# Optimization experiments

Hardware: AMD Instinct MI355X
Metric: run time of the kernel (lower is better)

Reference implementation:

```python
import jax, jax.numpy as jnp
import numpy as np

FP8_MAX = 448.0  # max representable magnitude of float8_e4m3fn


def _quantize_tensorwise(x):
    """Tensor-wise fp8 quantization. Returns (fp8 tensor, inverse_scale) where
    dequant = fp8.astype(f32) * inverse_scale (matches Fp8Quantization.quantize_tensorwise)."""
    amax = jnp.max(jnp.abs(x))
    inv_scale = jnp.maximum(amax / FP8_MAX, jnp.float32(1e-12))
    q = (x / inv_scale).astype(jnp.float8_e4m3fn)
    return q, inv_scale


def _fp8_mm(qa, qb, sa, sb):
    # scaled fp8 GEMM: accumulate in f32, apply product of per-tensor inverse scales
    return (qa.astype(jnp.float32) @ qb.astype(jnp.float32)) * (sa * sb)


def setup_inputs() -> dict:
    key = jax.random.key(0)
    k1, k2, k3 = jax.random.split(key, 3)
    x = jax.random.normal(k1, (4, 2048, 2048), dtype=jnp.float32)
    weight = jax.random.normal(k2, (2048, 2048), dtype=jnp.float32) * 0.02
    bias = jax.random.normal(k3, (2048,), dtype=jnp.float32) * 0.01
    return {"x": x, "weight": weight, "bias": bias}


def reference(x, weight, bias):
    # flatten leading dims: inputmat = input.view(-1, K)
    K = x.shape[-1]
    xm = x.reshape(-1, K)                      # [T, K]
    qx, sx = _quantize_tensorwise(xm)          # fp8 input + inverse scale
    qwt, swt = _quantize_tensorwise(weight.T)  # fp8 weight^T [K, N] + inverse scale
    out = _fp8_mm(qx, qwt, sx, swt) + bias     # [T, N]
    return out.reshape(*x.shape[:-1], -1)
```

## Files before the change

### kernel.cpp

```cpp
#include <hip/hip_runtime.h>
#include <stdint.h>

typedef float f32x4 __attribute__((ext_vector_type(4)));
typedef int   i32x4 __attribute__((ext_vector_type(4)));
typedef int   i32x8 __attribute__((ext_vector_type(8)));

__global__ __launch_bounds__(256) void amax2_kernel(
    const float* __restrict__ x, int nx4,
    const float* __restrict__ w, int nw4,
    int xblocks, int* __restrict__ out) {
  const float4* src;
  int n4, j0, stride, slot;
  if ((int)blockIdx.x < xblocks) {
    src = (const float4*)x; n4 = nx4; slot = 0;
    j0 = blockIdx.x * blockDim.x + threadIdx.x;
    stride = xblocks * blockDim.x;
  } else {
    src = (const float4*)w; n4 = nw4; slot = 1;
    j0 = (blockIdx.x - xblocks) * blockDim.x + threadIdx.x;
    stride = (gridDim.x - xblocks) * blockDim.x;
  }
  float m = 0.f;
  for (int j = j0; j < n4; j += stride) {
    float4 v = src[j];
    m = fmaxf(m, fmaxf(fmaxf(fabsf(v.x), fabsf(v.y)),
                       fmaxf(fabsf(v.z), fabsf(v.w))));
  }
#pragma unroll
  for (int off = 32; off; off >>= 1)
    m = fmaxf(m, __shfl_down(m, off, 64));
  __shared__ float red[4];
  const int lane = threadIdx.x & 63;
  const int wv = threadIdx.x >> 6;
  if (lane == 0) red[wv] = m;
  __syncthreads();
  if (threadIdx.x == 0) {
    m = fmaxf(fmaxf(red[0], red[1]), fmaxf(red[2], red[3]));
    atomicMax(out + slot, (int)__float_as_uint(m));
  }
}

__global__ __launch_bounds__(256) void quant2_kernel(
    const float* __restrict__ x, unsigned char* __restrict__ qx, int nx4,
    const float* __restrict__ w, unsigned char* __restrict__ qw, int nw4,
    int xblocks, const unsigned* __restrict__ amax2) {
  const float4* src;
  unsigned* dst;
  int n4, j0, stride;
  float amax;
  if ((int)blockIdx.x < xblocks) {
    src = (const float4*)x; dst = (unsigned*)qx; n4 = nx4;
    amax = __uint_as_float(amax2[0]);
    j0 = blockIdx.x * blockDim.x + threadIdx.x;
    stride = xblocks * blockDim.x;
  } else {
    src = (const float4*)w; dst = (unsigned*)qw; n4 = nw4;
    amax = __uint_as_float(amax2[1]);
    j0 = (blockIdx.x - xblocks) * blockDim.x + threadIdx.x;
    stride = (gridDim.x - xblocks) * blockDim.x;
  }
  const float inv_scale = fmaxf(amax / 448.0f, 1e-12f);
  for (int j = j0; j < n4; j += stride) {
    float4 v = src[j];
    float a0 = v.x / inv_scale;
    float a1 = v.y / inv_scale;
    float a2 = v.z / inv_scale;
    float a3 = v.w / inv_scale;
    int p = 0;
    p = __builtin_amdgcn_cvt_pk_fp8_f32(a0, a1, p, false);
    p = __builtin_amdgcn_cvt_pk_fp8_f32(a2, a3, p, true);
    dst[j] = (unsigned)p;
  }
}

#define BM 256
#define BN 256
#define BK 128
#define GEMM_LDS_BYTES (4 * 32768)

__device__ __forceinline__ void load_lds16(const void* g, void* l) {
  __builtin_amdgcn_global_load_lds(
      (const __attribute__((address_space(1))) unsigned int*)g,
      (__attribute__((address_space(3))) unsigned int*)l, 16, 0, 0);
}

__global__ __launch_bounds__(512, 2) void gemm_fp8_kernel(
    const unsigned char* __restrict__ Aq,
    const unsigned char* __restrict__ Bq,
    const float* __restrict__ bias,
    const unsigned* __restrict__ amax2,
    float* __restrict__ out,
    int T, int N, int K) {
  extern __shared__ unsigned char smem[];
  unsigned char* sA = smem;
  unsigned char* sB = smem + 65536;

  const int tid  = threadIdx.x;
  const int lane = tid & 63;
  const int wave = tid >> 6;
  const int wm = (wave >> 2) * 128;
  const int wn = (wave & 3) * 64;

  int lin = (int)(blockIdx.y * gridDim.x + blockIdx.x);
  const int nwg = (int)(gridDim.x * gridDim.y);
  if ((nwg & 7) == 0) lin = (lin & 7) * (nwg >> 3) + (lin >> 3);
  const long m0 = (long)(lin / (int)gridDim.x) * BM;
  const long n0 = (long)(lin % (int)gridDim.x) * BN;

  const long Kl = (long)K;

  const int row_s = tid >> 3;
  const int scol  = ((tid & 7) ^ (row_s & 7)) << 4;
  const int t16   = tid << 4;

  const int lm = lane & 15;
  const int qh = lane >> 4;
  const int c0 = ((qh * 2)     ^ (lm & 7)) << 4;
  const int c1 = ((qh * 2 + 1) ^ (lm & 7)) << 4;

  auto STAGE_A = [&](int Ts, int h) {
    const unsigned char* g = Aq + (m0 + h * 128 + row_s) * Kl + (long)Ts * BK + scol;
    unsigned char* l = sA + ((Ts & 1) << 15) + (h << 14) + t16;
    load_lds16(g, l);
    load_lds16(g + 64 * Kl, l + 8192);
  };
  auto STAGE_B = [&](int Ts, int h) {
    const unsigned char* g = Bq + (n0 + h * 128 + row_s) * Kl + (long)Ts * BK + scol;
    unsigned char* l = sB + ((Ts & 1) << 15) + (h << 14) + t16;
    load_lds16(g, l);
    load_lds16(g + 64 * Kl, l + 8192);
  };
  auto LDA = [&](const unsigned char* base, int mt) {
    const unsigned char* p = base + (wm + mt * 16 + lm) * BK;
    i32x4 lo = *(const i32x4*)(p + c0);
    i32x4 hi = *(const i32x4*)(p + c1);
    return (i32x8){lo.x, lo.y, lo.z, lo.w, hi.x, hi.y, hi.z, hi.w};
  };
  auto LDB = [&](const unsigned char* base, int nt) {
    const unsigned char* p = base + (wn + nt * 16 + lm) * BK;
    i32x4 lo = *(const i32x4*)(p + c0);
    i32x4 hi = *(const i32x4*)(p + c1);
    return (i32x8){lo.x, lo.y, lo.z, lo.w, hi.x, hi.y, hi.z, hi.w};
  };

  f32x4 acc[8][4];
#pragma unroll
  for (int i = 0; i < 8; ++i)
#pragma unroll
    for (int j = 0; j < 4; ++j) acc[i][j] = (f32x4){0.f, 0.f, 0.f, 0.f};

  const int nt = K / BK;

  STAGE_B(0, 0); STAGE_B(0, 1); STAGE_A(0, 0); STAGE_A(0, 1);
  STAGE_B(1, 0); STAGE_B(1, 1);
  asm volatile("s_waitcnt vmcnt(4)" ::: "memory");
  __builtin_amdgcn_s_barrier();

  i32x8 af[4], bf[4];
  for (int t = 0; t < nt; ++t) {
    const unsigned char* a = sA + ((t & 1) << 15);
    const unsigned char* b = sB + ((t & 1) << 15);

    af[0] = LDA(a, 0); af[1] = LDA(a, 1); af[2] = LDA(a, 2); af[3] = LDA(a, 3);
    bf[0] = LDB(b, 0); bf[1] = LDB(b, 1);
    if (t + 1 < nt) STAGE_A(t + 1, 0);
    __builtin_amdgcn_s_barrier();
    asm volatile("s_waitcnt lgkmcnt(0)");
    __builtin_amdgcn_sched_barrier(0);
    __builtin_amdgcn_s_setprio(1);
#pragma unroll
    for (int i = 0; i < 4; ++i)
#pragma unroll
      for (int j = 0; j < 2; ++j)
        acc[i][j] = __builtin_amdgcn_mfma_scale_f32_16x16x128_f8f6f4(
            af[i], bf[j], acc[i][j], 0, 0, 0, 0x7f7f7f7f, 0, 0x7f7f7f7f);
    __builtin_amdgcn_s_setprio(0);
    __builtin_amdgcn_s_barrier();

    bf[2] = LDB(b, 2); bf[3] = LDB(b, 3);
    if (t + 1 < nt) STAGE_A(t + 1, 1);
    __builtin_amdgcn_s_barrier();
    asm volatile("s_waitcnt lgkmcnt(0)");
    __builtin_amdgcn_sched_barrier(0);
    __builtin_amdgcn_s_setprio(1);
#pragma unroll
    for (int i = 0; i < 4; ++i)
#pragma unroll
      for (int j = 0; j < 2; ++j)
        acc[i][2 + j] = __builtin_amdgcn_mfma_scale_f32_16x16x128_f8f6f4(
            af[i], bf[2 + j], acc[i][2 + j], 0, 0, 0, 0x7f7f7f7f, 0, 0x7f7f7f7f);
    __builtin_amdgcn_s_setprio(0);
    __builtin_amdgcn_s_barrier();

    af[0] = LDA(a, 4); af[1] = LDA(a, 5); af[2] = LDA(a, 6); af[3] = LDA(a, 7);
    if (t + 2 < nt) STAGE_B(t + 2, 0);
    __builtin_amdgcn_s_barrier();
    asm volatile("s_waitcnt lgkmcnt(0)");
    __builtin_amdgcn_sched_barrier(0);
    __builtin_amdgcn_s_setprio(1);
#pragma unroll
    for (int i = 0; i < 4; ++i)
#pragma unroll
      for (int j = 0; j < 2; ++j)
        acc[4 + i][j] = __builtin_amdgcn_mfma_scale_f32_16x16x128_f8f6f4(
            af[i], bf[j], acc[4 + i][j], 0, 0, 0, 0x7f7f7f7f, 0, 0x7f7f7f7f);
    __builtin_amdgcn_s_setprio(0);
    __builtin_amdgcn_s_barrier();

    if (t + 2 < nt) STAGE_B(t + 2, 1);
    __builtin_amdgcn_s_setprio(1);
#pragma unroll
    for (int i = 0; i < 4; ++i)
#pragma unroll
      for (int j = 0; j < 2; ++j)
        acc[4 + i][2 + j] = __builtin_amdgcn_mfma_scale_f32_16x16x128_f8f6f4(
            af[i], bf[2 + j], acc[4 + i][2 + j], 0, 0, 0, 0x7f7f7f7f, 0, 0x7f7f7f7f);
    __builtin_amdgcn_s_setprio(0);
    asm volatile("s_waitcnt vmcnt(4)" ::: "memory");
    __builtin_amdgcn_s_barrier();
  }

  const float fsx = fmaxf(__uint_as_float(amax2[0]) / 448.0f, 1e-12f);
  const float fsw = fmaxf(__uint_as_float(amax2[1]) / 448.0f, 1e-12f);
  const float scale = fsx * fsw;
  const int rbase = qh * 4;
  float bv[4];
#pragma unroll
  for (int j = 0; j < 4; ++j) bv[j] = bias[n0 + wn + j * 16 + lm];
#pragma unroll
  for (int mt = 0; mt < 8; ++mt) {
#pragma unroll
    for (int r = 0; r < 4; ++r) {
      const long row = m0 + wm + mt * 16 + rbase + r;
      float* orow = out + row * (long)N + n0 + wn;
#pragma unroll
      for (int j = 0; j < 4; ++j)
        orow[j * 16 + lm] = acc[mt][j][r] * scale + bv[j];
    }
  }
}

extern "C" void kernel_launch(void* const* d_in, const int* in_sizes, int n_in,
                              void* d_out, int out_size, void* d_ws, size_t ws_size,
                              hipStream_t stream) {
  const float* x = (const float*)d_in[0];
  const float* w = (const float*)d_in[1];
  const float* bias = (const float*)d_in[2];
  float* out = (float*)d_out;

  const int N = in_sizes[2];
  const int K = in_sizes[1] / N;
  const int T = in_sizes[0] / K;

  unsigned* amax2 = (unsigned*)d_ws;
  unsigned char* qx = (unsigned char*)d_ws + 256;
  unsigned char* qw = qx + (size_t)T * K;

  const int XB = 1024;
  const int WB = 256;
  amax2_kernel<<<XB + WB, 256, 0, stream>>>(x, T * K / 4, w, N * K / 4, XB,
                                            (int*)amax2);
  quant2_kernel<<<XB + WB, 256, 0, stream>>>(x, qx, T * K / 4, w, qw, N * K / 4,
                                             XB, amax2);

  static bool lds_attr_set = false;
  if (!lds_attr_set) {
    (void)hipFuncSetAttribute((const void*)gemm_fp8_kernel,
                              hipFuncAttributeMaxDynamicSharedMemorySize,
                              GEMM_LDS_BYTES);
    lds_attr_set = true;
  }
  dim3 grid(N / BN, T / BM);
  gemm_fp8_kernel<<<grid, 512, GEMM_LDS_BYTES, stream>>>(qx, qw, bias, amax2,
                                                         out, T, N, K);
}
```

Baseline: 186.0 us.

## Software-pipeline LDS fragment reads with MFMA using register double buffering

The main loop is rebuilt so each of its four phases issues the LDS fragment reads for the next phase while running the MFMAs for the current one. A fragments now live in eight registers, and the first fragments of the next tile are prefetched from the other LDS buffer at the end of each iteration. Global-to-LDS staging is merged into whole-tile STAGE_A/STAGE_B calls with four loads each. Several waits on LDS reads after barriers are removed, at the cost of more live registers and a full vmcnt(0) drain once per iteration.

```diff
diff --git a/kernel.cpp b/kernel.cpp
--- a/kernel.cpp
+++ b/kernel.cpp
@@ -118,17 +118,21 @@
   const int c0 = ((qh * 2)     ^ (lm & 7)) << 4;
   const int c1 = ((qh * 2 + 1) ^ (lm & 7)) << 4;
 
-  auto STAGE_A = [&](int Ts, int h) {
-    const unsigned char* g = Aq + (m0 + h * 128 + row_s) * Kl + (long)Ts * BK + scol;
-    unsigned char* l = sA + ((Ts & 1) << 15) + (h << 14) + t16;
+  auto STAGE_A = [&](int Ts) {
+    const unsigned char* g = Aq + (m0 + row_s) * Kl + (long)Ts * BK + scol;
+    unsigned char* l = sA + ((Ts & 1) << 15) + t16;
     load_lds16(g, l);
-    load_lds16(g + 64 * Kl, l + 8192);
-  };
-  auto STAGE_B = [&](int Ts, int h) {
-    const unsigned char* g = Bq + (n0 + h * 128 + row_s) * Kl + (long)Ts * BK + scol;
-    unsigned char* l = sB + ((Ts & 1) << 15) + (h << 14) + t16;
+    load_lds16(g +  64 * Kl, l + 8192);
+    load_lds16(g + 128 * Kl, l + 16384);
+    load_lds16(g + 192 * Kl, l + 24576);
+  };
+  auto STAGE_B = [&](int Ts) {
+    const unsigned char* g = Bq + (n0 + row_s) * Kl + (long)Ts * BK + scol;
+    unsigned char* l = sB + ((Ts & 1) << 15) + t16;
     load_lds16(g, l);
-    load_lds16(g + 64 * Kl, l + 8192);
+    load_lds16(g +  64 * Kl, l + 8192);
+    load_lds16(g + 128 * Kl, l + 16384);
+    load_lds16(g + 192 * Kl, l + 24576);
   };
   auto LDA = [&](const unsigned char* base, int mt) {
     const unsigned char* p = base + (wm + mt * 16 + lm) * BK;
@@ -151,74 +155,77 @@
 
   const int nt = K / BK;
 
-  STAGE_B(0, 0); STAGE_B(0, 1); STAGE_A(0, 0); STAGE_A(0, 1);
-  STAGE_B(1, 0); STAGE_B(1, 1);
+  STAGE_A(0); STAGE_B(0);
+  STAGE_B(1);
   asm volatile("s_waitcnt vmcnt(4)" ::: "memory");
   __builtin_amdgcn_s_barrier();
 
-  i32x8 af[4], bf[4];
+  i32x8 af[8], bf[4];
+  af[0] = LDA(sA, 0); af[1] = LDA(sA, 1); af[2] = LDA(sA, 2); af[3] = LDA(sA, 3);
+  bf[0] = LDB(sB, 0); bf[1] = LDB(sB, 1);
+  STAGE_A(1);
+
+#define MFMA(ai, bj, ci, cj)                                            \
+  acc[ci][cj] = __builtin_amdgcn_mfma_scale_f32_16x16x128_f8f6f4(       \
+      af[ai], bf[bj], acc[ci][cj], 0, 0, 0, 0x7f7f7f7f, 0, 0x7f7f7f7f)
+
   for (int t = 0; t < nt; ++t) {
-    const unsigned char* a = sA + ((t & 1) << 15);
-    const unsigned char* b = sB + ((t & 1) << 15);
-
-    af[0] = LDA(a, 0); af[1] = LDA(a, 1); af[2] = LDA(a, 2); af[3] = LDA(a, 3);
-    bf[0] = LDB(b, 0); bf[1] = LDB(b, 1);
-    if (t + 1 < nt) STAGE_A(t + 1, 0);
-    __builtin_amdgcn_s_barrier();
-    asm volatile("s_waitcnt lgkmcnt(0)");
-    __builtin_amdgcn_sched_barrier(0);
-    __builtin_amdgcn_s_setprio(1);
-#pragma unroll
-    for (int i = 0; i < 4; ++i)
-#pragma unroll
-      for (int j = 0; j < 2; ++j)
-        acc[i][j] = __builtin_amdgcn_mfma_scale_f32_16x16x128_f8f6f4(
-            af[i], bf[j], acc[i][j], 0, 0, 0, 0x7f7f7f7f, 0, 0x7f7f7f7f);
-    __builtin_amdgcn_s_setprio(0);
-    __builtin_amdgcn_s_barrier();
-
+    const unsigned char* a  = sA + ((t & 1) << 15);
+    const unsigned char* b  = sB + ((t & 1) << 15);
+    const unsigned char* a1 = sA + (((t + 1) & 1) << 15);
+    const unsigned char* b1 = sB + (((t + 1) & 1) << 15);
+
+    asm volatile("s_waitcnt lgkmcnt(0)");
+    __builtin_amdgcn_sched_barrier(0);
+    __builtin_amdgcn_s_setprio(1);
     bf[2] = LDB(b, 2); bf[3] = LDB(b, 3);
-    if (t + 1 < nt) STAGE_A(t + 1, 1);
-    __builtin_amdgcn_s_barrier();
-    asm volatile("s_waitcnt lgkmcnt(0)");
-    __builtin_amdgcn_sched_barrier(0);
-    __builtin_amdgcn_s_setprio(1);
-#pragma unroll
-    for (int i = 0; i < 4; ++i)
-#pragma unroll
-      for (int j = 0; j < 2; ++j)
-        acc[i][2 + j] = __builtin_amdgcn_mfma_scale_f32_16x16x128_f8f6f4(
-            af[i], bf[2 + j], acc[i][2 + j], 0, 0, 0, 0x7f7f7f7f, 0, 0x7f7f7f7f);
-    __builtin_amdgcn_s_setprio(0);
-    __builtin_amdgcn_s_barrier();
-
-    af[0] = LDA(a, 4); af[1] = LDA(a, 5); af[2] = LDA(a, 6); af[3] = LDA(a, 7);
-    if (t + 2 < nt) STAGE_B(t + 2, 0);
-    __builtin_amdgcn_s_barrier();
-    asm volatile("s_waitcnt lgkmcnt(0)");
-    __builtin_amdgcn_sched_barrier(0);
-    __builtin_amdgcn_s_setprio(1);
-#pragma unroll
-    for (int i = 0; i < 4; ++i)
-#pragma unroll
-      for (int j = 0; j < 2; ++j)
-        acc[4 + i][j] = __builtin_amdgcn_mfma_scale_f32_16x16x128_f8f6f4(
-            af[i], bf[j], acc[4 + i][j], 0, 0, 0, 0x7f7f7f7f, 0, 0x7f7f7f7f);
-    __builtin_amdgcn_s_setprio(0);
-    __builtin_amdgcn_s_barrier();
-
-    if (t + 2 < nt) STAGE_B(t + 2, 1);
-    __builtin_amdgcn_s_setprio(1);
-#pragma unroll
-    for (int i = 0; i < 4; ++i)
-#pragma unroll
-      for (int j = 0; j < 2; ++j)
-        acc[4 + i][2 + j] = __builtin_amdgcn_mfma_scale_f32_16x16x128_f8f6f4(
-            af[i], bf[2 + j], acc[4 + i][2 + j], 0, 0, 0, 0x7f7f7f7f, 0, 0x7f7f7f7f);
-    __builtin_amdgcn_s_setprio(0);
-    asm volatile("s_waitcnt vmcnt(4)" ::: "memory");
-    __builtin_amdgcn_s_barrier();
-  }
+    MFMA(0, 0, 0, 0); MFMA(0, 1, 0, 1);
+    MFMA(1, 0, 1, 0); MFMA(1, 1, 1, 1);
+    MFMA(2, 0, 2, 0); MFMA(2, 1, 2, 1);
+    MFMA(3, 0, 3, 0); MFMA(3, 1, 3, 1);
+    __builtin_amdgcn_s_setprio(0);
+    __builtin_amdgcn_s_barrier();
+
+    asm volatile("s_waitcnt lgkmcnt(0)");
+    __builtin_amdgcn_sched_barrier(0);
+    __builtin_amdgcn_s_setprio(1);
+    af[4] = LDA(a, 4); af[5] = LDA(a, 5); af[6] = LDA(a, 6); af[7] = LDA(a, 7);
+    MFMA(0, 2, 0, 2); MFMA(0, 3, 0, 3);
+    MFMA(1, 2, 1, 2); MFMA(1, 3, 1, 3);
+    MFMA(2, 2, 2, 2); MFMA(2, 3, 2, 3);
+    MFMA(3, 2, 3, 2); MFMA(3, 3, 3, 3);
+    __builtin_amdgcn_s_setprio(0);
+    asm volatile("s_waitcnt vmcnt(0)" ::: "memory");
+    __builtin_amdgcn_s_barrier();
+
+    asm volatile("s_waitcnt lgkmcnt(0)");
+    __builtin_amdgcn_sched_barrier(0);
+    __builtin_amdgcn_s_setprio(1);
+    if (t + 1 < nt) {
+      af[0] = LDA(a1, 0); af[1] = LDA(a1, 1);
+      af[2] = LDA(a1, 2); af[3] = LDA(a1, 3);
+    }
+    if (t + 2 < nt) STAGE_B(t + 2);
+    MFMA(4, 0, 4, 0); MFMA(4, 1, 4, 1);
+    MFMA(5, 0, 5, 0); MFMA(5, 1, 5, 1);
+    MFMA(6, 0, 6, 0); MFMA(6, 1, 6, 1);
+    MFMA(7, 0, 7, 0); MFMA(7, 1, 7, 1);
+    __builtin_amdgcn_s_setprio(0);
+    __builtin_amdgcn_s_barrier();
+
+    asm volatile("s_waitcnt lgkmcnt(0)");
+    __builtin_amdgcn_sched_barrier(0);
+    __builtin_amdgcn_s_setprio(1);
+    if (t + 1 < nt) { bf[0] = LDB(b1, 0); bf[1] = LDB(b1, 1); }
+    if (t + 2 < nt) STAGE_A(t + 2);
+    MFMA(4, 2, 4, 2); MFMA(4, 3, 4, 3);
+    MFMA(5, 2, 5, 2); MFMA(5, 3, 5, 3);
+    MFMA(6, 2, 6, 2); MFMA(6, 3, 6, 3);
+    MFMA(7, 2, 7, 2); MFMA(7, 3, 7, 3);
+    __builtin_amdgcn_s_setprio(0);
+    __builtin_amdgcn_s_barrier();
+  }
+#undef MFMA
 
   const float fsx = fmaxf(__uint_as_float(amax2[0]) / 448.0f, 1e-12f);
   const float fsw = fmaxf(__uint_as_float(amax2[1]) / 448.0f, 1e-12f);
```

Measured after the change: 279.4 us. 1.5x slower.
